# Performance work log

Hardware: AMD Instinct MI355X
Metric: run time of the kernel (lower is better)

Reference implementation:

```python
import jax, jax.numpy as jnp
import numpy as np

B, LC, LT = 2, 1024, 1024
DS, DF = 2, 1
EOBS = 4                 # nn.Embed(2, 4)
D_IN = EOBS + DS + DF    # concat(obs, s, f)
EMB_H, D = 256, 64       # embed_obs_s_f = MLP([256, 64])
H, DH = 8, 8             # heads x head_dim = D
FFN_H = 128              # ffn = MLP([128, 64])
BIAS_H = 16              # DistanceBias hidden width
HEAD_H = 128             # head = MLP([128, 2])
NBLK = 6                 # num_blks (num_reps = 1)
EPS = 1e-6

def _ln(x, scale, bias):
    mu = jnp.mean(x, -1, keepdims=True)
    var = jnp.var(x, -1, keepdims=True)
    return (x - mu) * jax.lax.rsqrt(var + EPS) * scale + bias

def _mlp(x, w1, b1, w2, b2):
    return jax.nn.relu(x @ w1 + b1) @ w2 + b2

def _dist_bias(d, w1, b1, w2, b2):
    # d: [B, Lq, Lk] scalar distances -> per-head bias [B, H, Lq, Lk]
    h = jax.nn.relu(d[..., None] @ w1 + b1)
    return jnp.transpose(h @ w2 + b2, (0, 3, 1, 2))

def _mha(q_in, kv_in, wq, bq, wk, bk, wv, bv, wo, bo, bias):
    q = (q_in @ wq + bq).reshape(*q_in.shape[:-1], H, DH)
    k = (kv_in @ wk + bk).reshape(*kv_in.shape[:-1], H, DH)
    v = (kv_in @ wv + bv).reshape(*kv_in.shape[:-1], H, DH)
    scores = jnp.einsum('bqhd,bkhd->bhqk', q, k) / np.sqrt(DH).astype(np.float32) + bias
    a = jax.nn.softmax(scores, axis=-1)
    o = jnp.einsum('bhqk,bkhd->bqhd', a, v).reshape(*q_in.shape[:-1], D)
    return o @ wo + bo

def _forward(s_ctx, f_ctx, s_test, embed_obs_table, emb_w1, emb_b1, emb_w2, emb_b2,
             attn_wq, attn_bq, attn_wk, attn_bk, attn_wv, attn_bv, attn_wo, attn_bo,
             ffn_w1, ffn_b1, ffn_w2, ffn_b2, bias_w1, bias_b1, bias_w2, bias_b2,
             norm_scale, norm_bias, fnorm_scale, fnorm_bias,
             head_w1, head_b1, head_w2, head_b2):
    Bv, Lt = s_test.shape[0], s_test.shape[1]
    f_test = jnp.zeros((Bv, Lt, f_ctx.shape[-1]), f_ctx.dtype)
    obs = jnp.broadcast_to(embed_obs_table[1], (*f_ctx.shape[:-1], EOBS))
    unobs = jnp.broadcast_to(embed_obs_table[0], (Bv, Lt, EOBS))
    kvs = _mlp(jnp.concatenate([obs, s_ctx, f_ctx], -1), emb_w1, emb_b1, emb_w2, emb_b2)
    qvs = _mlp(jnp.concatenate([unobs, s_test, f_test], -1), emb_w1, emb_b1, emb_w2, emb_b2)
    # vmap(l2_dist_sq): pairwise squared L2 distances per batch element
    d_qk = jnp.sum((s_test[:, :, None, :] - s_ctx[:, None, :, :]) ** 2, -1)
    d_kk = jnp.sum((s_ctx[:, :, None, :] - s_ctx[:, None, :, :]) ** 2, -1)
    for i in range(NBLK):
        b_qk = _dist_bias(d_qk, bias_w1[i], bias_b1[i], bias_w2[i], bias_b2[i])
        b_kk = _dist_bias(d_kk, bias_w1[i], bias_b1[i], bias_w2[i], bias_b2[i])
        aw = (attn_wq[i], attn_bq[i], attn_wk[i], attn_bk[i], attn_wv[i], attn_bv[i], attn_wo[i], attn_bo[i])
        ns, nb = norm_scale[i], norm_bias[i]
        q_att = _ln(qvs + _mha(qvs, kvs, *aw, b_qk), ns, nb)
        k_att = _ln(kvs + _mha(kvs, kvs, *aw, b_kk), ns, nb)
        qvs = _ln(q_att + _mlp(q_att, ffn_w1[i], ffn_b1[i], ffn_w2[i], ffn_b2[i]), ns, nb)
        kvs = _ln(k_att + _mlp(k_att, ffn_w1[i], ffn_b1[i], ffn_w2[i], ffn_b2[i]), ns, nb)
    qvs = _ln(qvs, fnorm_scale, fnorm_bias)
    f_dist = _mlp(qvs, head_w1, head_b1, head_w2, head_b2)
    f_mu, f_log_var = jnp.split(f_dist, 2, axis=-1)
    f_std = jnp.exp(f_log_var / 2)  # min_std = 0.0
    return f_mu, f_std

def setup_inputs() -> dict:
    key = jax.random.key(0)
    ks = iter(jax.random.split(key, 40))
    r = lambda shp, s=0.05: jax.random.normal(next(ks), shp, jnp.float32) * s
    return dict(
        s_ctx=r((B, LC, DS), 1.0), f_ctx=r((B, LC, DF), 1.0), s_test=r((B, LT, DS), 1.0),
        embed_obs_table=r((2, EOBS)),
        emb_w1=r((D_IN, EMB_H)), emb_b1=jnp.zeros((EMB_H,)),
        emb_w2=r((EMB_H, D)), emb_b2=jnp.zeros((D,)),
        attn_wq=r((NBLK, D, D)), attn_bq=jnp.zeros((NBLK, D)),
        attn_wk=r((NBLK, D, D)), attn_bk=jnp.zeros((NBLK, D)),
        attn_wv=r((NBLK, D, D)), attn_bv=jnp.zeros((NBLK, D)),
        attn_wo=r((NBLK, D, D)), attn_bo=jnp.zeros((NBLK, D)),
        ffn_w1=r((NBLK, D, FFN_H)), ffn_b1=jnp.zeros((NBLK, FFN_H)),
        ffn_w2=r((NBLK, FFN_H, D)), ffn_b2=jnp.zeros((NBLK, D)),
        bias_w1=r((NBLK, 1, BIAS_H)), bias_b1=jnp.zeros((NBLK, BIAS_H)),
        bias_w2=r((NBLK, BIAS_H, H)), bias_b2=jnp.zeros((NBLK, H)),
        norm_scale=jnp.ones((NBLK, D)), norm_bias=jnp.zeros((NBLK, D)),
        fnorm_scale=jnp.ones((D,)), fnorm_bias=jnp.zeros((D,)),
        head_w1=r((D, HEAD_H)), head_b1=jnp.zeros((HEAD_H,)),
        head_w2=r((HEAD_H, 2)), head_b2=jnp.zeros((2,)),
    )

def reference(s_ctx, f_ctx, s_test, embed_obs_table, emb_w1, emb_b1, emb_w2, emb_b2,
              attn_wq, attn_bq, attn_wk, attn_bk, attn_wv, attn_bv, attn_wo, attn_bo,
              ffn_w1, ffn_b1, ffn_w2, ffn_b2, bias_w1, bias_b1, bias_w2, bias_b2,
              norm_scale, norm_bias, fnorm_scale, fnorm_bias,
              head_w1, head_b1, head_w2, head_b2):
    return _forward(s_ctx, f_ctx, s_test, embed_obs_table, emb_w1, emb_b1, emb_w2, emb_b2,
                    attn_wq, attn_bq, attn_wk, attn_bk, attn_wv, attn_bv, attn_wo, attn_bo,
                    ffn_w1, ffn_b1, ffn_w2, ffn_b2, bias_w1, bias_b1, bias_w2, bias_b2,
                    norm_scale, norm_bias, fnorm_scale, fnorm_bias,
                    head_w1, head_b1, head_w2, head_b2)
```

## Files before the change

### kernel.cpp

```cpp
#include <hip/hip_runtime.h>
#include <hip/hip_bf16.h>

typedef __hip_bfloat16 bf16;
typedef float v2f __attribute__((ext_vector_type(2)));

#define LEN 1024
#define N2 2048
#define SCALE_L2E 0.5100697918f

#define I_SCTX   0
#define I_FCTX   4096
#define I_STEST  6144
#define I_OBS    10240
#define I_EW1    10248
#define I_EB1    12040
#define I_EW2    12296
#define I_EB2    28680
#define I_WQ     28744
#define I_BQ     53320
#define I_WK     53704
#define I_BK     78280
#define I_WV     78664
#define I_BV     103240
#define I_WO     103624
#define I_BO     128200
#define I_FW1    128584
#define I_FB1    177736
#define I_FW2    178504
#define I_FB2    227656
#define I_BW1    228040
#define I_BB1    228136
#define I_BW2    228232
#define I_BB2    229000
#define I_NS     229048
#define I_NB     229432
#define I_FNS    229816
#define I_FNB    229880
#define I_HW1    229944
#define I_HB1    238136
#define I_HW2    238264
#define I_HB2    238520

#define OFF_PW   240256
#define OFF_QVS  262144
#define OFF_KVS  393216
#define OFF_Q1   524288
#define OFF_Q2   655360
#define OFF_KB   786432
#define OFF_VB   917504
#define OFF_PART 1048576
#define PART_KS  196608

__constant__ int C_OFFS[33] = {
    0, 4096, 6144, 10240, 10248, 12040, 12296, 28680, 28744, 53320, 53704,
    78280, 78664, 103240, 103624, 128200, 128584, 177736, 178504, 227656,
    228040, 228136, 228232, 229000, 229048, 229432, 229816, 229880, 229944,
    238136, 238264, 238520, 238522 };

struct InPtrs { const void* p[32]; };

__device__ __forceinline__ float pack2(float a, float b) {
    __hip_bfloat16 ha = __float2bfloat16(a), hb = __float2bfloat16(b);
    unsigned ua = *(unsigned short*)&ha, ub = *(unsigned short*)&hb;
    return __uint_as_float(ua | (ub << 16));
}
__device__ __forceinline__ float unlo(float f) {
    return __uint_as_float(__float_as_uint(f) << 16);
}
__device__ __forceinline__ float unhi(float f) {
    return __uint_as_float(__float_as_uint(f) & 0xffff0000u);
}

__global__ __launch_bounds__(256) void k_cvt(InPtrs ptrs, float* ws) {
    const unsigned u0 = *(const unsigned*)ptrs.p[24];
    const int isbf = (u0 == 0x3F803F80u);
    const int i = blockIdx.y;
    const int o0 = C_OFFS[i], n = C_OFFS[i + 1] - o0;
    const void* src = ptrs.p[i];
    for (int j = blockIdx.x * 256 + threadIdx.x; j < n; j += gridDim.x * 256) {
        float v = isbf ? __bfloat162float(((const bf16*)src)[j])
                       : ((const float*)src)[j];
        ws[o0 + j] = v;
    }
}

__global__ __launch_bounds__(256) void k_pw(float* ws) {
    const int L = blockIdx.x, t = threadIdx.x;
    __shared__ float w1s[16], b1s[16], bps[16];
    __shared__ int rnk[16];
    if (t < 16) {
        float w = ws[I_BW1 + L * 16 + t], b0 = ws[I_BB1 + L * 16 + t];
        w1s[t] = w; b1s[t] = b0;
        bps[t] = (w != 0.f) ? (-b0 / w) : 1e30f;
    }
    __syncthreads();
    if (t < 16) {
        float me = bps[t]; int r = 0;
        for (int j = 0; j < 16; ++j) {
            float o = bps[j];
            if (o < me || (o == me && j < t)) ++r;
        }
        rnk[t] = r;
    }
    __syncthreads();
    if (t < 16) ws[OFF_PW + L * 288 + 272 + rnk[t]] = bps[t];
    if (t < 136) {
        int s = t >> 3, h = t & 7;
        float slope = 0.f, inter = ws[I_BB2 + L * 8 + h];
        for (int j = 0; j < 16; ++j) {
            float w = w1s[j];
            bool act = (w > 0.f) ? (rnk[j] < s)
                     : (w < 0.f) ? (rnk[j] >= s)
                                 : (b1s[j] > 0.f);
            if (act) {
                float w2v = ws[I_BW2 + L * 128 + j * 8 + h];
                slope += w * w2v;
                inter += b1s[j] * w2v;
            }
        }
        const float LOG2E = 1.4426950408889634f;
        ws[OFF_PW + L * 288 + (s * 8 + h) * 2]     = slope * LOG2E;
        ws[OFF_PW + L * 288 + (s * 8 + h) * 2 + 1] = inter * LOG2E;
    }
}

__global__ __launch_bounds__(256) void k_embed(float* ws) {
    __shared__ float hbuf[256];
    __shared__ float red[256];
    int r = blockIdx.x, t = threadIdx.x;
    bool is_ctx = (r < N2);
    int rr = is_ctx ? r : r - N2;
    const float* ob = ws + I_OBS + (is_ctx ? 4 : 0);
    const float* s  = ws + (is_ctx ? I_SCTX : I_STEST);
    float in[7];
    in[0] = ob[0]; in[1] = ob[1]; in[2] = ob[2]; in[3] = ob[3];
    in[4] = s[rr * 2]; in[5] = s[rr * 2 + 1];
    in[6] = is_ctx ? ws[I_FCTX + rr] : 0.f;

    float acc = ws[I_EB1 + t];
#pragma unroll
    for (int i = 0; i < 7; ++i) acc += in[i] * ws[I_EW1 + i * 256 + t];
    hbuf[t] = fmaxf(acc, 0.f);
    __syncthreads();

    int d = t & 63, p = t >> 6;
    float a2 = 0.f;
#pragma unroll 8
    for (int j = p * 64; j < p * 64 + 64; ++j) a2 += hbuf[j] * ws[I_EW2 + j * 64 + d];
    red[t] = a2;
    __syncthreads();
    if (t < 64) {
        float o = red[t] + red[64 + t] + red[128 + t] + red[192 + t] + ws[I_EB2 + t];
        float* dst = ws + (is_ctx ? OFF_KVS : OFF_QVS);
        dst[rr * 64 + t] = o;
    }
}

__global__ __launch_bounds__(256) void k_qkv(int blk, float* ws) {
    __shared__ float xs[2][64];
    int r = blockIdx.x, t = threadIdx.x;
    if (t < 64)       xs[0][t] = ws[OFF_QVS + r * 64 + t];
    else if (t < 128) xs[1][t - 64] = ws[OFF_KVS + r * 64 + (t - 64)];
    __syncthreads();
    int o = t >> 6, d = t & 63;
    const float* x = (o == 0) ? xs[0] : xs[1];
    const float* W; const float* bb; float* dst;
    if (o <= 1)      { W = ws + I_WQ + blk * 4096; bb = ws + I_BQ + blk * 64; dst = ws + (o == 0 ? OFF_Q1 : OFF_Q2); }
    else if (o == 2) { W = ws + I_WK + blk * 4096; bb = ws + I_BK + blk * 64; dst = ws + OFF_KB; }
    else             { W = ws + I_WV + blk * 4096; bb = ws + I_BV + blk * 64; dst = ws + OFF_VB; }
    float acc = bb[d];
#pragma unroll 8
    for (int k = 0; k < 64; ++k) acc += x[k] * W[k * 64 + d];
    dst[r * 64 + d] = acc;
}

__global__ __launch_bounds__(256, 7) void k_attn(int blk, float* ws) {
    __shared__ float Ks[2176];
    __shared__ float Vs[2176];
    __shared__ float Sds[544];
    __shared__ v2f   pw[136];

    const int t = threadIdx.x;
    const int qt = blockIdx.x, ks = blockIdx.y, z = blockIdx.z;
    const int b = z & 1, kind = z >> 1;
    const int q0 = qt * 16;
    const float* Qbuf = ws + (kind == 0 ? OFF_Q1 : OFF_Q2);
    const float* Kbuf = ws + OFF_KB;
    const float* Vbuf = ws + OFF_VB;
    const float* sq_src = ws + (kind == 0 ? I_STEST : I_SCTX);
    const float* sk_src = ws + I_SCTX;
    const float* pwg = ws + OFF_PW + blk * 288;

    float bp[16];
#pragma unroll
    for (int j = 0; j < 16; ++j) bp[j] = pwg[272 + j];

    if (t < 136) pw[t] = (v2f){ pwg[t * 2], pwg[t * 2 + 1] };

    const int q2 = t >> 4, h2 = (t >> 1) & 7, par = t & 1;
    const int tk = t & 15;

    v2f qf[4];
    {
        const float* qp = Qbuf + (b * LEN + q0 + q2) * 64 + h2 * 8;
        float4 qa = *(const float4*)qp;
        float4 qb = *(const float4*)(qp + 4);
        qf[0] = (v2f){qa.x, qa.y}; qf[1] = (v2f){qa.z, qa.w};
        qf[2] = (v2f){qb.x, qb.y}; qf[3] = (v2f){qb.z, qb.w};
    }
    float sqx, sqy;
    {
        const float* sp = sq_src + (b * LEN + q0 + q2) * 2;
        sqx = sp[0]; sqy = sp[1];
    }

    float m = -1e30f, lsum = 0.f;
    v2f oacc[4] = {};

    for (int kt = ks * 4; kt < ks * 4 + 4; ++kt) {
        __syncthreads();
        {
            int kr = t >> 3, j = (t & 7) * 8;
            const float* ksrc = Kbuf + (b * LEN + kt * 32 + kr) * 64 + j;
            const float* vsrc = Vbuf + (b * LEN + kt * 32 + kr) * 64 + j;
            *(float4*)&Ks[kr * 68 + j]     = *(const float4*)ksrc;
            *(float4*)&Ks[kr * 68 + j + 4] = *(const float4*)(ksrc + 4);
            *(float4*)&Vs[kr * 68 + j]     = *(const float4*)vsrc;
            *(float4*)&Vs[kr * 68 + j + 4] = *(const float4*)(vsrc + 4);
        }
        {
            float4 kc = *(const float4*)(sk_src + (b * LEN + kt * 32 + tk * 2) * 2);
            float dx0 = sqx - kc.x, dy0 = sqy - kc.y;
            float dx1 = sqx - kc.z, dy1 = sqy - kc.w;
            float d0 = dx0 * dx0 + dy0 * dy0;
            float d1 = dx1 * dx1 + dy1 * dy1;
            int s0 = 0, s1 = 0;
#pragma unroll
            for (int j = 0; j < 16; ++j) { s0 += (d0 > bp[j]); s1 += (d1 > bp[j]); }
            Sds[(tk * 2) * 17 + q2]     = __uint_as_float((__float_as_uint(d0) & ~31u) | s0);
            Sds[(tk * 2 + 1) * 17 + q2] = __uint_as_float((__float_as_uint(d1) & ~31u) | s1);
        }
        __syncthreads();

        float sv[16];
#pragma unroll
        for (int j = 0; j < 16; ++j) {
            int k = par + 2 * j;
            unsigned u = __float_as_uint(Sds[k * 17 + q2]);
            float dv = __uint_as_float(u & ~31u);
            v2f pv_ = pw[(u & 31u) * 8 + h2];
            const v2f* kf = (const v2f*)&Ks[k * 68 + h2 * 8];
            v2f acc = qf[0] * kf[0];
            acc += qf[1] * kf[1];
            acc += qf[2] * kf[2];
            acc += qf[3] * kf[3];
            sv[j] = (acc.x + acc.y) * SCALE_L2E + (pv_.x * dv + pv_.y);
        }
        float tm = m;
#pragma unroll
        for (int j = 0; j < 16; ++j) tm = fmaxf(tm, sv[j]);
        float alpha = exp2f(m - tm);
        lsum *= alpha;
        v2f av = (v2f){alpha, alpha};
#pragma unroll
        for (int c = 0; c < 4; ++c) oacc[c] *= av;
#pragma unroll
        for (int j = 0; j < 16; ++j) {
            int k = par + 2 * j;
            float p = exp2f(sv[j] - tm);
            lsum += p;
            const v2f* vf = (const v2f*)&Vs[k * 68 + h2 * 8];
            v2f pp = (v2f){p, p};
            oacc[0] += pp * vf[0];
            oacc[1] += pp * vf[1];
            oacc[2] += pp * vf[2];
            oacc[3] += pp * vf[3];
        }
        m = tm;
    }

    {
        float mo = __shfl_xor(m, 1);
        float Mx = fmaxf(m, mo);
        float a0 = exp2f(m - Mx), a1 = exp2f(mo - Mx);
        float lo = __shfl_xor(lsum, 1);
        float Lt = lsum * a0 + lo * a1;
        float ov[8];
#pragma unroll
        for (int c = 0; c < 4; ++c) {
            v2f x = oacc[c];
            ov[2 * c]     = x.x * a0 + __shfl_xor(x.x, 1) * a1;
            ov[2 * c + 1] = x.y * a0 + __shfl_xor(x.y, 1) * a1;
        }
        if (par == 0) {
            float inv = 1.f / Lt;
            float lse = Mx + log2f(Lt);
            float* p = ws + OFF_PART + ks * PART_KS + ((z * LEN + q0 + q2) * 8 + h2) * 6;
            *(v2f*)(p)     = (v2f){ pack2(ov[0] * inv, ov[1] * inv), pack2(ov[2] * inv, ov[3] * inv) };
            *(v2f*)(p + 2) = (v2f){ pack2(ov[4] * inv, ov[5] * inv), pack2(ov[6] * inv, ov[7] * inv) };
            *(v2f*)(p + 4) = (v2f){ lse, 0.f };
        }
    }
}

__global__ __launch_bounds__(256) void k_fuse(int blk, float* ws, const void* ns_raw, void* out_raw) {
    __shared__ float xo[8 * 68];
    __shared__ float xsm[8 * 68];
    __shared__ float hs[8 * 132];
    __shared__ float xn[8 * 68];
    const int t = threadIdx.x;
    const int kind = blockIdx.y;
    const int r0 = blockIdx.x * 8;
    float* io = ws + (kind == 0 ? OFF_QVS : OFF_KVS);

    {
        int r = t >> 5, h = (t >> 2) & 7, q = t & 3;
        int rg = r0 + r, b = rg >> 10, row = rg & 1023, z = kind * 2 + b;
        const float* e0 = ws + OFF_PART + q * PART_KS + ((z * LEN + row) * 8 + h) * 6;
        const float* e1 = e0 + 4 * PART_KS;
        v2f a0 = *(const v2f*)e0, a1 = *(const v2f*)(e0 + 2), a2 = *(const v2f*)(e0 + 4);
        v2f c0 = *(const v2f*)e1, c1 = *(const v2f*)(e1 + 2), c2 = *(const v2f*)(e1 + 4);
        float M = fmaxf(a2.x, c2.x);
        M = fmaxf(M, __shfl_xor(M, 1));
        M = fmaxf(M, __shfl_xor(M, 2));
        float wA = exp2f(a2.x - M), wB = exp2f(c2.x - M);
        float den = wA + wB;
        float num[8];
        num[0] = wA * unlo(a0.x) + wB * unlo(c0.x);
        num[1] = wA * unhi(a0.x) + wB * unhi(c0.x);
        num[2] = wA * unlo(a0.y) + wB * unlo(c0.y);
        num[3] = wA * unhi(a0.y) + wB * unhi(c0.y);
        num[4] = wA * unlo(a1.x) + wB * unlo(c1.x);
        num[5] = wA * unhi(a1.x) + wB * unhi(c1.x);
        num[6] = wA * unlo(a1.y) + wB * unlo(c1.y);
        num[7] = wA * unhi(a1.y) + wB * unhi(c1.y);
        den += __shfl_xor(den, 1); den += __shfl_xor(den, 2);
#pragma unroll
        for (int d_ = 0; d_ < 8; ++d_) {
            num[d_] += __shfl_xor(num[d_], 1);
            num[d_] += __shfl_xor(num[d_], 2);
        }
        float invd = 1.f / den;
        xo[r * 68 + h * 8 + 2 * q]     = num[2 * q] * invd;
        xo[r * 68 + h * 8 + 2 * q + 1] = num[2 * q + 1] * invd;
    }
    __syncthreads();

    const int r = t >> 5, dd = (t & 31) * 2;
    const int rg = r0 + r;
    float xs0, xs1;

    {
        const float* Wo = ws + I_WO + blk * 4096;
        v2f acc = *(const v2f*)(ws + I_BO + blk * 64 + dd);
#pragma unroll 8
        for (int k = 0; k < 64; ++k) {
            float xv = xo[r * 68 + k];
            v2f w = *(const v2f*)(Wo + k * 64 + dd);
            acc.x += xv * w.x; acc.y += xv * w.y;
        }
        v2f rv = *(const v2f*)(io + rg * 64 + dd);
        acc.x += rv.x; acc.y += rv.y;
        float s = acc.x + acc.y, s2 = acc.x * acc.x + acc.y * acc.y;
#pragma unroll
        for (int off = 1; off < 32; off <<= 1) { s += __shfl_xor(s, off); s2 += __shfl_xor(s2, off); }
        float mu = s * (1.f / 64.f);
        float var = s2 * (1.f / 64.f) - mu * mu;
        float rs = rsqrtf(fmaxf(var, 0.f) + 1e-6f);
        v2f nsv = *(const v2f*)(ws + I_NS + blk * 64 + dd);
        v2f nbv = *(const v2f*)(ws + I_NB + blk * 64 + dd);
        xs0 = (acc.x - mu) * rs * nsv.x + nbv.x;
        xs1 = (acc.y - mu) * rs * nsv.y + nbv.y;
        *(v2f*)&xsm[r * 68 + dd] = (v2f){xs0, xs1};
    }
    __syncthreads();

    {
        int rc = t >> 5, c4 = (t & 31) * 4;
        const float* W1 = ws + I_FW1 + blk * 8192;
        float4 acc = *(const float4*)(ws + I_FB1 + blk * 128 + c4);
#pragma unroll 4
        for (int k = 0; k < 64; ++k) {
            float xv = xsm[rc * 68 + k];
            float4 w = *(const float4*)(W1 + k * 128 + c4);
            acc.x += xv * w.x; acc.y += xv * w.y; acc.z += xv * w.z; acc.w += xv * w.w;
        }
        acc.x = fmaxf(acc.x, 0.f); acc.y = fmaxf(acc.y, 0.f);
        acc.z = fmaxf(acc.z, 0.f); acc.w = fmaxf(acc.w, 0.f);
        *(float4*)&hs[rc * 132 + c4] = acc;
    }
    __syncthreads();

    float v0, v1;
    {
        const float* W2 = ws + I_FW2 + blk * 8192;
        v2f acc = *(const v2f*)(ws + I_FB2 + blk * 64 + dd);
#pragma unroll 8
        for (int k = 0; k < 128; ++k) {
            float hv = hs[r * 132 + k];
            v2f w = *(const v2f*)(W2 + k * 64 + dd);
            acc.x += hv * w.x; acc.y += hv * w.y;
        }
        acc.x += xs0; acc.y += xs1;
        float s = acc.x + acc.y, s2 = acc.x * acc.x + acc.y * acc.y;
#pragma unroll
        for (int off = 1; off < 32; off <<= 1) { s += __shfl_xor(s, off); s2 += __shfl_xor(s2, off); }
        float mu = s * (1.f / 64.f);
        float var = s2 * (1.f / 64.f) - mu * mu;
        float rs = rsqrtf(fmaxf(var, 0.f) + 1e-6f);
        v2f nsv = *(const v2f*)(ws + I_NS + blk * 64 + dd);
        v2f nbv = *(const v2f*)(ws + I_NB + blk * 64 + dd);
        v0 = (acc.x - mu) * rs * nsv.x + nbv.x;
        v1 = (acc.y - mu) * rs * nsv.y + nbv.y;
        *(v2f*)(io + rg * 64 + dd) = (v2f){v0, v1};
        *(v2f*)&xn[r * 68 + dd] = (v2f){v0, v1};
    }
    __syncthreads();

    if (blk < 5) {
        const int nb_ = blk + 1;
        if (kind == 0) {
            const float* WQ = ws + I_WQ + nb_ * 4096;
            v2f acc = *(const v2f*)(ws + I_BQ + nb_ * 64 + dd);
#pragma unroll 8
            for (int k = 0; k < 64; ++k) {
                float xv = xn[r * 68 + k];
                v2f w = *(const v2f*)(WQ + k * 64 + dd);
                acc.x += xv * w.x; acc.y += xv * w.y;
            }
            *(v2f*)(ws + OFF_Q1 + rg * 64 + dd) = acc;
        } else {
            const float* WQ = ws + I_WQ + nb_ * 4096;
            const float* WK = ws + I_WK + nb_ * 4096;
            const float* WV = ws + I_WV + nb_ * 4096;
            v2f aq = *(const v2f*)(ws + I_BQ + nb_ * 64 + dd);
            v2f ak = *(const v2f*)(ws + I_BK + nb_ * 64 + dd);
            v2f av = *(const v2f*)(ws + I_BV + nb_ * 64 + dd);
#pragma unroll 4
            for (int k = 0; k < 64; ++k) {
                float xv = xn[r * 68 + k];
                v2f wq = *(const v2f*)(WQ + k * 64 + dd);
                v2f wk = *(const v2f*)(WK + k * 64 + dd);
                v2f wv = *(const v2f*)(WV + k * 64 + dd);
                aq.x += xv * wq.x; aq.y += xv * wq.y;
                ak.x += xv * wk.x; ak.y += xv * wk.y;
                av.x += xv * wv.x; av.y += xv * wv.y;
            }
            *(v2f*)(ws + OFF_Q2 + rg * 64 + dd) = aq;
            *(v2f*)(ws + OFF_KB + rg * 64 + dd) = ak;
            *(v2f*)(ws + OFF_VB + rg * 64 + dd) = av;
        }
    } else if (kind == 0) {
        {
            float s = v0 + v1, s2 = v0 * v0 + v1 * v1;
#pragma unroll
            for (int off = 1; off < 32; off <<= 1) { s += __shfl_xor(s, off); s2 += __shfl_xor(s2, off); }
            float mu = s * (1.f / 64.f);
            float var = s2 * (1.f / 64.f) - mu * mu;
            float rs = rsqrtf(fmaxf(var, 0.f) + 1e-6f);
            v2f fns = *(const v2f*)(ws + I_FNS + dd);
            v2f fnb = *(const v2f*)(ws + I_FNB + dd);
            *(v2f*)&xsm[r * 68 + dd] = (v2f){ (v0 - mu) * rs * fns.x + fnb.x,
                                              (v1 - mu) * rs * fns.y + fnb.y };
        }
        __syncthreads();
        {
            int rc = t >> 5, c4 = (t & 31) * 4;
            const float* W1 = ws + I_HW1;
            float4 acc = *(const float4*)(ws + I_HB1 + c4);
#pragma unroll 4
            for (int k = 0; k < 64; ++k) {
                float xv = xsm[rc * 68 + k];
                float4 w = *(const float4*)(W1 + k * 128 + c4);
                acc.x += xv * w.x; acc.y += xv * w.y; acc.z += xv * w.z; acc.w += xv * w.w;
            }
            acc.x = fmaxf(acc.x, 0.f); acc.y = fmaxf(acc.y, 0.f);
            acc.z = fmaxf(acc.z, 0.f); acc.w = fmaxf(acc.w, 0.f);
            *(float4*)&hs[rc * 132 + c4] = acc;
        }
        __syncthreads();
        if (t < 16) {
            int rr = t >> 1, c = t & 1;
            float a = ws[I_HB2 + c];
            for (int k = 0; k < 128; ++k) a += hs[rr * 132 + k] * ws[I_HW2 + k * 2 + c];
            float v = c ? exp2f(a * 0.7213475204444817f) : a;
            int rgg = r0 + rr;
            int idx = c ? (N2 + rgg) : rgg;
            unsigned u0 = *(const unsigned*)ns_raw;
            if (u0 == 0x3F803F80u) ((bf16*)out_raw)[idx] = __float2bfloat16(v);
            else                   ((float*)out_raw)[idx] = v;
        }
    }
}

extern "C" void kernel_launch(void* const* d_in, const int* in_sizes, int n_in,
                              void* d_out, int out_size, void* d_ws, size_t ws_size,
                              hipStream_t stream) {
    float* ws = (float*)d_ws;

    InPtrs ptrs;
    for (int i = 0; i < 32; ++i) ptrs.p[i] = d_in[i];

    k_cvt<<<dim3(8, 32), 256, 0, stream>>>(ptrs, ws);
    k_pw<<<6, 256, 0, stream>>>(ws);
    k_embed<<<4096, 256, 0, stream>>>(ws);
    k_qkv<<<2048, 256, 0, stream>>>(0, ws);
    for (int i = 0; i < 6; ++i) {
        k_attn<<<dim3(64, 8, 4), 256, 0, stream>>>(i, ws);
        k_fuse<<<dim3(256, 2), 256, 0, stream>>>(i, ws, d_in[24], d_out);
    }
}
```

Baseline: 604.5 us.

## Register-tile attention over four query rows per thread and halve fuse block rows

Attention threads now each own four query rows and split the 32-key tile eight ways instead of two. Each K and V row loaded from LDS is then reused across four queries, and the cross-lane softmax merge grows to three shuffle stages. Partial outputs are staged in shared memory and written back as coalesced float4 stores. The fuse kernel drops to 128 threads and 4 rows per block with twice as many blocks. In exchange, register pressure rises, so the attention launch bound is relaxed from 7 to 4 waves, which may reduce occupancy.

```diff
diff --git a/kernel.cpp b/kernel.cpp
--- a/kernel.cpp
+++ b/kernel.cpp
@@ -174,7 +174,7 @@
     dst[r * 64 + d] = acc;
 }
 
-__global__ __launch_bounds__(256, 7) void k_attn(int blk, float* ws) {
+__global__ __launch_bounds__(256, 4) void k_attn(int blk, float* ws) {
     __shared__ float Ks[2176];
     __shared__ float Vs[2176];
     __shared__ float Sds[544];
@@ -197,25 +197,27 @@
 
     if (t < 136) pw[t] = (v2f){ pwg[t * 2], pwg[t * 2 + 1] };
 
-    const int q2 = t >> 4, h2 = (t >> 1) & 7, par = t & 1;
-    const int tk = t & 15;
-
-    v2f qf[4];
+    const int par = t & 7, h2 = (t >> 3) & 7, q4 = t >> 6;
+    const int pq = t >> 4, pk = t & 15;
+    float sqx, sqy;
     {
-        const float* qp = Qbuf + (b * LEN + q0 + q2) * 64 + h2 * 8;
+        const float* sp = sq_src + (b * LEN + q0 + pq) * 2;
+        sqx = sp[0]; sqy = sp[1];
+    }
+
+    v2f qf[4][4];
+#pragma unroll
+    for (int i = 0; i < 4; ++i) {
+        const float* qp = Qbuf + (b * LEN + q0 + q4 + 4 * i) * 64 + h2 * 8;
         float4 qa = *(const float4*)qp;
         float4 qb = *(const float4*)(qp + 4);
-        qf[0] = (v2f){qa.x, qa.y}; qf[1] = (v2f){qa.z, qa.w};
-        qf[2] = (v2f){qb.x, qb.y}; qf[3] = (v2f){qb.z, qb.w};
-    }
-    float sqx, sqy;
-    {
-        const float* sp = sq_src + (b * LEN + q0 + q2) * 2;
-        sqx = sp[0]; sqy = sp[1];
-    }
-
-    float m = -1e30f, lsum = 0.f;
-    v2f oacc[4] = {};
+        qf[i][0] = (v2f){qa.x, qa.y}; qf[i][1] = (v2f){qa.z, qa.w};
+        qf[i][2] = (v2f){qb.x, qb.y}; qf[i][3] = (v2f){qb.z, qb.w};
+    }
+
+    float m[4] = {-1e30f, -1e30f, -1e30f, -1e30f};
+    float l[4] = {};
+    v2f oacc[4][4] = {};
 
     for (int kt = ks * 4; kt < ks * 4 + 4; ++kt) {
         __syncthreads();
@@ -229,7 +231,7 @@
             *(float4*)&Vs[kr * 68 + j + 4] = *(const float4*)(vsrc + 4);
         }
         {
-            float4 kc = *(const float4*)(sk_src + (b * LEN + kt * 32 + tk * 2) * 2);
+            float4 kc = *(const float4*)(sk_src + (b * LEN + kt * 32 + pk * 2) * 2);
             float dx0 = sqx - kc.x, dy0 = sqy - kc.y;
             float dx1 = sqx - kc.z, dy1 = sqy - kc.w;
             float d0 = dx0 * dx0 + dy0 * dy0;
@@ -237,80 +239,114 @@
             int s0 = 0, s1 = 0;
 #pragma unroll
             for (int j = 0; j < 16; ++j) { s0 += (d0 > bp[j]); s1 += (d1 > bp[j]); }
-            Sds[(tk * 2) * 17 + q2]     = __uint_as_float((__float_as_uint(d0) & ~31u) | s0);
-            Sds[(tk * 2 + 1) * 17 + q2] = __uint_as_float((__float_as_uint(d1) & ~31u) | s1);
+            Sds[(pk * 2) * 17 + pq]     = __uint_as_float((__float_as_uint(d0) & ~31u) | s0);
+            Sds[(pk * 2 + 1) * 17 + pq] = __uint_as_float((__float_as_uint(d1) & ~31u) | s1);
         }
         __syncthreads();
 
         float sv[16];
 #pragma unroll
-        for (int j = 0; j < 16; ++j) {
-            int k = par + 2 * j;
-            unsigned u = __float_as_uint(Sds[k * 17 + q2]);
-            float dv = __uint_as_float(u & ~31u);
-            v2f pv_ = pw[(u & 31u) * 8 + h2];
+        for (int j = 0; j < 4; ++j) {
+            int k = par + 8 * j;
             const v2f* kf = (const v2f*)&Ks[k * 68 + h2 * 8];
-            v2f acc = qf[0] * kf[0];
-            acc += qf[1] * kf[1];
-            acc += qf[2] * kf[2];
-            acc += qf[3] * kf[3];
-            sv[j] = (acc.x + acc.y) * SCALE_L2E + (pv_.x * dv + pv_.y);
-        }
-        float tm = m;
-#pragma unroll
-        for (int j = 0; j < 16; ++j) tm = fmaxf(tm, sv[j]);
-        float alpha = exp2f(m - tm);
-        lsum *= alpha;
-        v2f av = (v2f){alpha, alpha};
-#pragma unroll
-        for (int c = 0; c < 4; ++c) oacc[c] *= av;
-#pragma unroll
-        for (int j = 0; j < 16; ++j) {
-            int k = par + 2 * j;
-            float p = exp2f(sv[j] - tm);
-            lsum += p;
+            v2f k0 = kf[0], k1 = kf[1], k2 = kf[2], k3 = kf[3];
+#pragma unroll
+            for (int i = 0; i < 4; ++i) {
+                unsigned u = __float_as_uint(Sds[k * 17 + q4 + 4 * i]);
+                float dv = __uint_as_float(u & ~31u);
+                v2f pv_ = pw[(u & 31u) * 8 + h2];
+                v2f acc = qf[i][0] * k0;
+                acc += qf[i][1] * k1;
+                acc += qf[i][2] * k2;
+                acc += qf[i][3] * k3;
+                sv[i * 4 + j] = (acc.x + acc.y) * SCALE_L2E + (pv_.x * dv + pv_.y);
+            }
+        }
+#pragma unroll
+        for (int i = 0; i < 4; ++i) {
+            float tm = m[i];
+#pragma unroll
+            for (int j = 0; j < 4; ++j) tm = fmaxf(tm, sv[i * 4 + j]);
+            float alpha = exp2f(m[i] - tm);
+            l[i] *= alpha;
+            v2f av = (v2f){alpha, alpha};
+#pragma unroll
+            for (int c = 0; c < 4; ++c) oacc[i][c] *= av;
+            m[i] = tm;
+#pragma unroll
+            for (int j = 0; j < 4; ++j) {
+                float p = exp2f(sv[i * 4 + j] - tm);
+                sv[i * 4 + j] = p;
+                l[i] += p;
+            }
+        }
+#pragma unroll
+        for (int j = 0; j < 4; ++j) {
+            int k = par + 8 * j;
             const v2f* vf = (const v2f*)&Vs[k * 68 + h2 * 8];
-            v2f pp = (v2f){p, p};
-            oacc[0] += pp * vf[0];
-            oacc[1] += pp * vf[1];
-            oacc[2] += pp * vf[2];
-            oacc[3] += pp * vf[3];
-        }
-        m = tm;
-    }
-
-    {
-        float mo = __shfl_xor(m, 1);
-        float Mx = fmaxf(m, mo);
-        float a0 = exp2f(m - Mx), a1 = exp2f(mo - Mx);
-        float lo = __shfl_xor(lsum, 1);
-        float Lt = lsum * a0 + lo * a1;
-        float ov[8];
-#pragma unroll
-        for (int c = 0; c < 4; ++c) {
-            v2f x = oacc[c];
-            ov[2 * c]     = x.x * a0 + __shfl_xor(x.x, 1) * a1;
-            ov[2 * c + 1] = x.y * a0 + __shfl_xor(x.y, 1) * a1;
-        }
-        if (par == 0) {
-            float inv = 1.f / Lt;
-            float lse = Mx + log2f(Lt);
-            float* p = ws + OFF_PART + ks * PART_KS + ((z * LEN + q0 + q2) * 8 + h2) * 6;
-            *(v2f*)(p)     = (v2f){ pack2(ov[0] * inv, ov[1] * inv), pack2(ov[2] * inv, ov[3] * inv) };
-            *(v2f*)(p + 2) = (v2f){ pack2(ov[4] * inv, ov[5] * inv), pack2(ov[6] * inv, ov[7] * inv) };
-            *(v2f*)(p + 4) = (v2f){ lse, 0.f };
-        }
-    }
-}
-
-__global__ __launch_bounds__(256) void k_fuse(int blk, float* ws, const void* ns_raw, void* out_raw) {
-    __shared__ float xo[8 * 68];
-    __shared__ float xsm[8 * 68];
-    __shared__ float hs[8 * 132];
-    __shared__ float xn[8 * 68];
+            v2f v0 = vf[0], v1 = vf[1], v2 = vf[2], v3 = vf[3];
+#pragma unroll
+            for (int i = 0; i < 4; ++i) {
+                float p = sv[i * 4 + j];
+                v2f pp = (v2f){p, p};
+                oacc[i][0] += pp * v0;
+                oacc[i][1] += pp * v1;
+                oacc[i][2] += pp * v2;
+                oacc[i][3] += pp * v3;
+            }
+        }
+    }
+
+#pragma unroll
+    for (int st = 1; st <= 4; st <<= 1) {
+#pragma unroll
+        for (int i = 0; i < 4; ++i) {
+            float mo = __shfl_xor(m[i], st);
+            float Mx = fmaxf(m[i], mo);
+            float a0 = exp2f(m[i] - Mx), a1 = exp2f(mo - Mx);
+            float lo = __shfl_xor(l[i], st);
+            l[i] = l[i] * a0 + lo * a1;
+#pragma unroll
+            for (int c = 0; c < 4; ++c) {
+                v2f x = oacc[i][c];
+                float x0 = x.x * a0 + __shfl_xor(x.x, st) * a1;
+                float x1 = x.y * a0 + __shfl_xor(x.y, st) * a1;
+                oacc[i][c] = (v2f){x0, x1};
+            }
+            m[i] = Mx;
+        }
+    }
+
+    __syncthreads();
+    float* stg = Ks;
+    if (par == 0) {
+#pragma unroll
+        for (int i = 0; i < 4; ++i) {
+            float inv = 1.f / l[i];
+            float lse = m[i] + log2f(l[i]);
+            float* p = &stg[(q4 + 4 * i) * 48 + h2 * 6];
+            p[0] = pack2(oacc[i][0].x * inv, oacc[i][0].y * inv);
+            p[1] = pack2(oacc[i][1].x * inv, oacc[i][1].y * inv);
+            p[2] = pack2(oacc[i][2].x * inv, oacc[i][2].y * inv);
+            p[3] = pack2(oacc[i][3].x * inv, oacc[i][3].y * inv);
+            p[4] = lse; p[5] = 0.f;
+        }
+    }
+    __syncthreads();
+    if (t < 192) {
+        float* dst = ws + OFF_PART + ks * PART_KS + (z * LEN + q0) * 48;
+        *(float4*)(dst + t * 4) = *(const float4*)(stg + t * 4);
+    }
+}
+
+__global__ __launch_bounds__(128) void k_fuse(int blk, float* ws, const void* ns_raw, void* out_raw) {
+    __shared__ float xo[4 * 68];
+    __shared__ float xsm[4 * 68];
+    __shared__ float hs[4 * 132];
+    __shared__ float xn[4 * 68];
     const int t = threadIdx.x;
     const int kind = blockIdx.y;
-    const int r0 = blockIdx.x * 8;
+    const int r0 = blockIdx.x * 4;
     float* io = ws + (kind == 0 ? OFF_QVS : OFF_KVS);
 
     {
@@ -479,7 +515,7 @@
             *(float4*)&hs[rc * 132 + c4] = acc;
         }
         __syncthreads();
-        if (t < 16) {
+        if (t < 8) {
             int rr = t >> 1, c = t & 1;
             float a = ws[I_HB2 + c];
             for (int k = 0; k < 128; ++k) a += hs[rr * 132 + k] * ws[I_HW2 + k * 2 + c];
@@ -507,6 +543,6 @@
     k_qkv<<<2048, 256, 0, stream>>>(0, ws);
     for (int i = 0; i < 6; ++i) {
         k_attn<<<dim3(64, 8, 4), 256, 0, stream>>>(i, ws);
-        k_fuse<<<dim3(256, 2), 256, 0, stream>>>(i, ws, d_in[24], d_out);
-    }
-}
+        k_fuse<<<dim3(512, 2), 128, 0, stream>>>(i, ws, d_in[24], d_out);
+    }
+}
```

New measurement: 634.3 us. 4.9% more time.

## Rebalance attention key splits to six and halve rows per fuse block

Applied to the files above, without the earlier changes.

The attention kernel now splits the 32 key tiles into 6 uneven chunks (6,6,5,5,5,5) instead of 8 chunks of 4, cutting grid size. Partial outputs are stored in a per-row contiguous layout so the fuse kernel can load all six partials with coalesced float4 loads into shared memory before merging them. The fuse kernel processes 4 rows per block with one thread per output column, which doubles its grid and drops the vector-pair layout. Fewer key splits reduce merge traffic but lower attention parallelism.

```diff
diff --git a/kernel.cpp b/kernel.cpp
--- a/kernel.cpp
+++ b/kernel.cpp
@@ -49,7 +49,6 @@
 #define OFF_KB   786432
 #define OFF_VB   917504
 #define OFF_PART 1048576
-#define PART_KS  196608
 
 __constant__ int C_OFFS[33] = {
     0, 4096, 6144, 10240, 10248, 12040, 12296, 28680, 28744, 53320, 53704,
@@ -198,7 +197,12 @@
     if (t < 136) pw[t] = (v2f){ pwg[t * 2], pwg[t * 2 + 1] };
 
     const int q2 = t >> 4, h2 = (t >> 1) & 7, par = t & 1;
-    const int tk = t & 15;
+    const int pq = t >> 4, pk = t & 15;
+    float sqx, sqy;
+    {
+        const float* sp = sq_src + (b * LEN + q0 + pq) * 2;
+        sqx = sp[0]; sqy = sp[1];
+    }
 
     v2f qf[4];
     {
@@ -208,16 +212,13 @@
         qf[0] = (v2f){qa.x, qa.y}; qf[1] = (v2f){qa.z, qa.w};
         qf[2] = (v2f){qb.x, qb.y}; qf[3] = (v2f){qb.z, qb.w};
     }
-    float sqx, sqy;
-    {
-        const float* sp = sq_src + (b * LEN + q0 + q2) * 2;
-        sqx = sp[0]; sqy = sp[1];
-    }
 
     float m = -1e30f, lsum = 0.f;
     v2f oacc[4] = {};
 
-    for (int kt = ks * 4; kt < ks * 4 + 4; ++kt) {
+    const int kt0 = ks * 5 + (ks < 2 ? ks : 2);
+    const int ktn = (ks < 2) ? 6 : 5;
+    for (int kt = kt0; kt < kt0 + ktn; ++kt) {
         __syncthreads();
         {
             int kr = t >> 3, j = (t & 7) * 8;
@@ -229,7 +230,7 @@
             *(float4*)&Vs[kr * 68 + j + 4] = *(const float4*)(vsrc + 4);
         }
         {
-            float4 kc = *(const float4*)(sk_src + (b * LEN + kt * 32 + tk * 2) * 2);
+            float4 kc = *(const float4*)(sk_src + (b * LEN + kt * 32 + pk * 2) * 2);
             float dx0 = sqx - kc.x, dy0 = sqy - kc.y;
             float dx1 = sqx - kc.z, dy1 = sqy - kc.w;
             float d0 = dx0 * dx0 + dy0 * dy0;
@@ -237,8 +238,8 @@
             int s0 = 0, s1 = 0;
 #pragma unroll
             for (int j = 0; j < 16; ++j) { s0 += (d0 > bp[j]); s1 += (d1 > bp[j]); }
-            Sds[(tk * 2) * 17 + q2]     = __uint_as_float((__float_as_uint(d0) & ~31u) | s0);
-            Sds[(tk * 2 + 1) * 17 + q2] = __uint_as_float((__float_as_uint(d1) & ~31u) | s1);
+            Sds[(pk * 2) * 17 + pq]     = __uint_as_float((__float_as_uint(d0) & ~31u) | s0);
+            Sds[(pk * 2 + 1) * 17 + pq] = __uint_as_float((__float_as_uint(d1) & ~31u) | s1);
         }
         __syncthreads();
 
@@ -295,125 +296,105 @@
         if (par == 0) {
             float inv = 1.f / Lt;
             float lse = Mx + log2f(Lt);
-            float* p = ws + OFF_PART + ks * PART_KS + ((z * LEN + q0 + q2) * 8 + h2) * 6;
-            *(v2f*)(p)     = (v2f){ pack2(ov[0] * inv, ov[1] * inv), pack2(ov[2] * inv, ov[3] * inv) };
-            *(v2f*)(p + 2) = (v2f){ pack2(ov[4] * inv, ov[5] * inv), pack2(ov[6] * inv, ov[7] * inv) };
-            *(v2f*)(p + 4) = (v2f){ lse, 0.f };
+            float* p = ws + OFF_PART + (z * LEN + q0 + q2) * 384 + (h2 * 6 + ks) * 8;
+            *(float4*)(p)     = make_float4(pack2(ov[0] * inv, ov[1] * inv),
+                                            pack2(ov[2] * inv, ov[3] * inv),
+                                            pack2(ov[4] * inv, ov[5] * inv),
+                                            pack2(ov[6] * inv, ov[7] * inv));
+            *(float4*)(p + 4) = make_float4(lse, 0.f, 0.f, 0.f);
         }
     }
 }
 
 __global__ __launch_bounds__(256) void k_fuse(int blk, float* ws, const void* ns_raw, void* out_raw) {
-    __shared__ float xo[8 * 68];
-    __shared__ float xsm[8 * 68];
-    __shared__ float hs[8 * 132];
-    __shared__ float xn[8 * 68];
+    __shared__ float raw[1536];
+    __shared__ float xo[256];
+    __shared__ float xsm[256];
+    __shared__ float hs[512];
+    __shared__ float xn[256];
     const int t = threadIdx.x;
     const int kind = blockIdx.y;
-    const int r0 = blockIdx.x * 8;
+    const int r0 = blockIdx.x * 4;
+    const int bq_ = r0 >> 10;
+    const int z = kind * 2 + bq_;
+    const int row0 = r0 & 1023;
     float* io = ws + (kind == 0 ? OFF_QVS : OFF_KVS);
 
     {
-        int r = t >> 5, h = (t >> 2) & 7, q = t & 3;
-        int rg = r0 + r, b = rg >> 10, row = rg & 1023, z = kind * 2 + b;
-        const float* e0 = ws + OFF_PART + q * PART_KS + ((z * LEN + row) * 8 + h) * 6;
-        const float* e1 = e0 + 4 * PART_KS;
-        v2f a0 = *(const v2f*)e0, a1 = *(const v2f*)(e0 + 2), a2 = *(const v2f*)(e0 + 4);
-        v2f c0 = *(const v2f*)e1, c1 = *(const v2f*)(e1 + 2), c2 = *(const v2f*)(e1 + 4);
-        float M = fmaxf(a2.x, c2.x);
-        M = fmaxf(M, __shfl_xor(M, 1));
-        M = fmaxf(M, __shfl_xor(M, 2));
-        float wA = exp2f(a2.x - M), wB = exp2f(c2.x - M);
-        float den = wA + wB;
-        float num[8];
-        num[0] = wA * unlo(a0.x) + wB * unlo(c0.x);
-        num[1] = wA * unhi(a0.x) + wB * unhi(c0.x);
-        num[2] = wA * unlo(a0.y) + wB * unlo(c0.y);
-        num[3] = wA * unhi(a0.y) + wB * unhi(c0.y);
-        num[4] = wA * unlo(a1.x) + wB * unlo(c1.x);
-        num[5] = wA * unhi(a1.x) + wB * unhi(c1.x);
-        num[6] = wA * unlo(a1.y) + wB * unlo(c1.y);
-        num[7] = wA * unhi(a1.y) + wB * unhi(c1.y);
-        den += __shfl_xor(den, 1); den += __shfl_xor(den, 2);
-#pragma unroll
-        for (int d_ = 0; d_ < 8; ++d_) {
-            num[d_] += __shfl_xor(num[d_], 1);
-            num[d_] += __shfl_xor(num[d_], 2);
-        }
-        float invd = 1.f / den;
-        xo[r * 68 + h * 8 + 2 * q]     = num[2 * q] * invd;
-        xo[r * 68 + h * 8 + 2 * q + 1] = num[2 * q + 1] * invd;
-    }
-    __syncthreads();
-
-    const int r = t >> 5, dd = (t & 31) * 2;
+        const float* pbase = ws + OFF_PART + (z * LEN + row0) * 384;
+        for (int i = t; i < 384; i += 256)
+            ((float4*)raw)[i] = ((const float4*)pbase)[i];
+    }
+    __syncthreads();
+    {
+        int r = t >> 6, h = (t >> 3) & 7, d = t & 7;
+        const float* e = raw + r * 384 + h * 48;
+        float M = -1e30f;
+#pragma unroll
+        for (int k2 = 0; k2 < 6; ++k2) M = fmaxf(M, e[k2 * 8 + 4]);
+        float den = 0.f, num = 0.f;
+#pragma unroll
+        for (int k2 = 0; k2 < 6; ++k2) {
+            float w = exp2f(e[k2 * 8 + 4] - M);
+            den += w;
+            float pf = e[k2 * 8 + (d >> 1)];
+            num += w * ((d & 1) ? unhi(pf) : unlo(pf));
+        }
+        xo[r * 64 + h * 8 + d] = num / den;
+    }
+    __syncthreads();
+
+    const int r = t >> 6, c = t & 63;
     const int rg = r0 + r;
-    float xs0, xs1;
+    float xs_;
 
     {
         const float* Wo = ws + I_WO + blk * 4096;
-        v2f acc = *(const v2f*)(ws + I_BO + blk * 64 + dd);
-#pragma unroll 8
-        for (int k = 0; k < 64; ++k) {
-            float xv = xo[r * 68 + k];
-            v2f w = *(const v2f*)(Wo + k * 64 + dd);
-            acc.x += xv * w.x; acc.y += xv * w.y;
-        }
-        v2f rv = *(const v2f*)(io + rg * 64 + dd);
-        acc.x += rv.x; acc.y += rv.y;
-        float s = acc.x + acc.y, s2 = acc.x * acc.x + acc.y * acc.y;
-#pragma unroll
-        for (int off = 1; off < 32; off <<= 1) { s += __shfl_xor(s, off); s2 += __shfl_xor(s2, off); }
+        float a = ws[I_BO + blk * 64 + c];
+#pragma unroll 8
+        for (int k = 0; k < 64; ++k) a += xo[r * 64 + k] * Wo[k * 64 + c];
+        a += io[rg * 64 + c];
+        float s = a, s2 = a * a;
+#pragma unroll
+        for (int off = 1; off < 64; off <<= 1) { s += __shfl_xor(s, off); s2 += __shfl_xor(s2, off); }
         float mu = s * (1.f / 64.f);
         float var = s2 * (1.f / 64.f) - mu * mu;
         float rs = rsqrtf(fmaxf(var, 0.f) + 1e-6f);
-        v2f nsv = *(const v2f*)(ws + I_NS + blk * 64 + dd);
-        v2f nbv = *(const v2f*)(ws + I_NB + blk * 64 + dd);
-        xs0 = (acc.x - mu) * rs * nsv.x + nbv.x;
-        xs1 = (acc.y - mu) * rs * nsv.y + nbv.y;
-        *(v2f*)&xsm[r * 68 + dd] = (v2f){xs0, xs1};
-    }
-    __syncthreads();
-
-    {
-        int rc = t >> 5, c4 = (t & 31) * 4;
+        xs_ = (a - mu) * rs * ws[I_NS + blk * 64 + c] + ws[I_NB + blk * 64 + c];
+        xsm[r * 64 + c] = xs_;
+    }
+    __syncthreads();
+
+    {
         const float* W1 = ws + I_FW1 + blk * 8192;
-        float4 acc = *(const float4*)(ws + I_FB1 + blk * 128 + c4);
-#pragma unroll 4
+        float a0 = ws[I_FB1 + blk * 128 + c], a1 = ws[I_FB1 + blk * 128 + c + 64];
+#pragma unroll 8
         for (int k = 0; k < 64; ++k) {
-            float xv = xsm[rc * 68 + k];
-            float4 w = *(const float4*)(W1 + k * 128 + c4);
-            acc.x += xv * w.x; acc.y += xv * w.y; acc.z += xv * w.z; acc.w += xv * w.w;
-        }
-        acc.x = fmaxf(acc.x, 0.f); acc.y = fmaxf(acc.y, 0.f);
-        acc.z = fmaxf(acc.z, 0.f); acc.w = fmaxf(acc.w, 0.f);
-        *(float4*)&hs[rc * 132 + c4] = acc;
-    }
-    __syncthreads();
-
-    float v0, v1;
+            float x = xsm[r * 64 + k];
+            a0 += x * W1[k * 128 + c];
+            a1 += x * W1[k * 128 + c + 64];
+        }
+        hs[r * 128 + c] = fmaxf(a0, 0.f);
+        hs[r * 128 + c + 64] = fmaxf(a1, 0.f);
+    }
+    __syncthreads();
+
+    float v_;
     {
         const float* W2 = ws + I_FW2 + blk * 8192;
-        v2f acc = *(const v2f*)(ws + I_FB2 + blk * 64 + dd);
-#pragma unroll 8
-        for (int k = 0; k < 128; ++k) {
-            float hv = hs[r * 132 + k];
-            v2f w = *(const v2f*)(W2 + k * 64 + dd);
-            acc.x += hv * w.x; acc.y += hv * w.y;
-        }
-        acc.x += xs0; acc.y += xs1;
-        float s = acc.x + acc.y, s2 = acc.x * acc.x + acc.y * acc.y;
-#pragma unroll
-        for (int off = 1; off < 32; off <<= 1) { s += __shfl_xor(s, off); s2 += __shfl_xor(s2, off); }
+        float a = ws[I_FB2 + blk * 64 + c];
+#pragma unroll 8
+        for (int k = 0; k < 128; ++k) a += hs[r * 128 + k] * W2[k * 64 + c];
+        a += xs_;
+        float s = a, s2 = a * a;
+#pragma unroll
+        for (int off = 1; off < 64; off <<= 1) { s += __shfl_xor(s, off); s2 += __shfl_xor(s2, off); }
         float mu = s * (1.f / 64.f);
         float var = s2 * (1.f / 64.f) - mu * mu;
         float rs = rsqrtf(fmaxf(var, 0.f) + 1e-6f);
-        v2f nsv = *(const v2f*)(ws + I_NS + blk * 64 + dd);
-        v2f nbv = *(const v2f*)(ws + I_NB + blk * 64 + dd);
-        v0 = (acc.x - mu) * rs * nsv.x + nbv.x;
-        v1 = (acc.y - mu) * rs * nsv.y + nbv.y;
-        *(v2f*)(io + rg * 64 + dd) = (v2f){v0, v1};
-        *(v2f*)&xn[r * 68 + dd] = (v2f){v0, v1};
+        v_ = (a - mu) * rs * ws[I_NS + blk * 64 + c] + ws[I_NB + blk * 64 + c];
+        io[rg * 64 + c] = v_;
+        xn[r * 64 + c] = v_;
     }
     __syncthreads();
 
@@ -421,71 +402,59 @@
         const int nb_ = blk + 1;
         if (kind == 0) {
             const float* WQ = ws + I_WQ + nb_ * 4096;
-            v2f acc = *(const v2f*)(ws + I_BQ + nb_ * 64 + dd);
-#pragma unroll 8
-            for (int k = 0; k < 64; ++k) {
-                float xv = xn[r * 68 + k];
-                v2f w = *(const v2f*)(WQ + k * 64 + dd);
-                acc.x += xv * w.x; acc.y += xv * w.y;
-            }
-            *(v2f*)(ws + OFF_Q1 + rg * 64 + dd) = acc;
+            float a = ws[I_BQ + nb_ * 64 + c];
+#pragma unroll 8
+            for (int k = 0; k < 64; ++k) a += xn[r * 64 + k] * WQ[k * 64 + c];
+            ws[OFF_Q1 + rg * 64 + c] = a;
         } else {
             const float* WQ = ws + I_WQ + nb_ * 4096;
             const float* WK = ws + I_WK + nb_ * 4096;
             const float* WV = ws + I_WV + nb_ * 4096;
-            v2f aq = *(const v2f*)(ws + I_BQ + nb_ * 64 + dd);
-            v2f ak = *(const v2f*)(ws + I_BK + nb_ * 64 + dd);
-            v2f av = *(const v2f*)(ws + I_BV + nb_ * 64 + dd);
+            float aq = ws[I_BQ + nb_ * 64 + c];
+            float ak = ws[I_BK + nb_ * 64 + c];
+            float av = ws[I_BV + nb_ * 64 + c];
 #pragma unroll 4
             for (int k = 0; k < 64; ++k) {
-                float xv = xn[r * 68 + k];
-                v2f wq = *(const v2f*)(WQ + k * 64 + dd);
-                v2f wk = *(const v2f*)(WK + k * 64 + dd);
-                v2f wv = *(const v2f*)(WV + k * 64 + dd);
-                aq.x += xv * wq.x; aq.y += xv * wq.y;
-                ak.x += xv * wk.x; ak.y += xv * wk.y;
-                av.x += xv * wv.x; av.y += xv * wv.y;
+                float x = xn[r * 64 + k];
+                aq += x * WQ[k * 64 + c];
+                ak += x * WK[k * 64 + c];
+                av += x * WV[k * 64 + c];
             }
-            *(v2f*)(ws + OFF_Q2 + rg * 64 + dd) = aq;
-            *(v2f*)(ws + OFF_KB + rg * 64 + dd) = ak;
-            *(v2f*)(ws + OFF_VB + rg * 64 + dd) = av;
+            ws[OFF_Q2 + rg * 64 + c] = aq;
+            ws[OFF_KB + rg * 64 + c] = ak;
+            ws[OFF_VB + rg * 64 + c] = av;
         }
     } else if (kind == 0) {
         {
-            float s = v0 + v1, s2 = v0 * v0 + v1 * v1;
-#pragma unroll
-            for (int off = 1; off < 32; off <<= 1) { s += __shfl_xor(s, off); s2 += __shfl_xor(s2, off); }
+            float s = v_, s2 = v_ * v_;
+#pragma unroll
+            for (int off = 1; off < 64; off <<= 1) { s += __shfl_xor(s, off); s2 += __shfl_xor(s2, off); }
             float mu = s * (1.f / 64.f);
             float var = s2 * (1.f / 64.f) - mu * mu;
             float rs = rsqrtf(fmaxf(var, 0.f) + 1e-6f);
-            v2f fns = *(const v2f*)(ws + I_FNS + dd);
-            v2f fnb = *(const v2f*)(ws + I_FNB + dd);
-            *(v2f*)&xsm[r * 68 + dd] = (v2f){ (v0 - mu) * rs * fns.x + fnb.x,
-                                              (v1 - mu) * rs * fns.y + fnb.y };
+            xsm[r * 64 + c] = (v_ - mu) * rs * ws[I_FNS + c] + ws[I_FNB + c];
         }
         __syncthreads();
         {
-            int rc = t >> 5, c4 = (t & 31) * 4;
             const float* W1 = ws + I_HW1;
-            float4 acc = *(const float4*)(ws + I_HB1 + c4);
-#pragma unroll 4
+            float a0 = ws[I_HB1 + c], a1 = ws[I_HB1 + c + 64];
+#pragma unroll 8
             for (int k = 0; k < 64; ++k) {
-                float xv = xsm[rc * 68 + k];
-                float4 w = *(const float4*)(W1 + k * 128 + c4);
-                acc.x += xv * w.x; acc.y += xv * w.y; acc.z += xv * w.z; acc.w += xv * w.w;
+                float x = xsm[r * 64 + k];
+                a0 += x * W1[k * 128 + c];
+                a1 += x * W1[k * 128 + c + 64];
             }
-            acc.x = fmaxf(acc.x, 0.f); acc.y = fmaxf(acc.y, 0.f);
-            acc.z = fmaxf(acc.z, 0.f); acc.w = fmaxf(acc.w, 0.f);
-            *(float4*)&hs[rc * 132 + c4] = acc;
+            hs[r * 128 + c] = fmaxf(a0, 0.f);
+            hs[r * 128 + c + 64] = fmaxf(a1, 0.f);
         }
         __syncthreads();
-        if (t < 16) {
-            int rr = t >> 1, c = t & 1;
-            float a = ws[I_HB2 + c];
-            for (int k = 0; k < 128; ++k) a += hs[rr * 132 + k] * ws[I_HW2 + k * 2 + c];
-            float v = c ? exp2f(a * 0.7213475204444817f) : a;
+        if (t < 8) {
+            int rr = t >> 1, cb = t & 1;
+            float a = ws[I_HB2 + cb];
+            for (int k = 0; k < 128; ++k) a += hs[rr * 128 + k] * ws[I_HW2 + k * 2 + cb];
+            float v = cb ? exp2f(a * 0.7213475204444817f) : a;
             int rgg = r0 + rr;
-            int idx = c ? (N2 + rgg) : rgg;
+            int idx = cb ? (N2 + rgg) : rgg;
             unsigned u0 = *(const unsigned*)ns_raw;
             if (u0 == 0x3F803F80u) ((bf16*)out_raw)[idx] = __float2bfloat16(v);
             else                   ((float*)out_raw)[idx] = v;
@@ -506,7 +475,7 @@
     k_embed<<<4096, 256, 0, stream>>>(ws);
     k_qkv<<<2048, 256, 0, stream>>>(0, ws);
     for (int i = 0; i < 6; ++i) {
-        k_attn<<<dim3(64, 8, 4), 256, 0, stream>>>(i, ws);
-        k_fuse<<<dim3(256, 2), 256, 0, stream>>>(i, ws, d_in[24], d_out);
-    }
-}
+        k_attn<<<dim3(64, 6, 4), 256, 0, stream>>>(i, ws);
+        k_fuse<<<dim3(512, 2), 256, 0, stream>>>(i, ws, d_in[24], d_out);
+    }
+}
```

Result: faster. 553.9 us (-8.4%).
